# Performance work log

Measured on AMD Instinct MI355X. Metric: run time of the kernel, lower is better.

Reference implementation:

```python
import jax, jax.numpy as jnp
import numpy as np

B, N, D, H = 64, 196, 768, 3072
QMAX = 127.0  # 8-bit symmetric: clamp to [-128, 127]


def ste_round(x):
    # straight-through-estimator round (QAT)
    return x + jax.lax.stop_gradient(jnp.round(x) - x)


def q_linear_diag(x, w, b, a_sf):
    """Quantized diagonal linear (ResMLP Affine / LayerScale as QuantLinear)."""
    w_sf = jnp.max(jnp.abs(w)) / QMAX            # per-tensor weight scale
    w_int = ste_round(w / w_sf)                  # int8 weights (|.|<=127)
    out_int = (x / a_sf) * w_int
    if b is not None:
        out_int = out_int + ste_round(b / (a_sf * w_sf))  # 32-bit bias
    return out_int * (a_sf * w_sf), w_sf


def q_linear_dense(x, w, b, a_sf):
    """Quantized dense linear: int8 GEMM + int32 bias, dequant with a_sf*w_sf."""
    w_sf = jnp.max(jnp.abs(w)) / QMAX
    w_int = jnp.clip(ste_round(w / w_sf), -QMAX - 1, QMAX)
    out_int = jnp.einsum('...i,oi->...o', x / a_sf, w_int) + ste_round(b / (a_sf * w_sf))
    return out_int * (a_sf * w_sf), w_sf


def q_act(x, pre_sf, new_sf, identity=None, id_sf=None):
    """HAWQ-style QuantAct: fixed-point requantization to scale new_sf (8-bit)."""
    if identity is None:
        z_int = ste_round(x / pre_sf)
        out_int = ste_round(z_int * (pre_sf / new_sf))
    else:
        # main branch (x - identity) requantized with pre_sf, identity with id_sf
        z_int = ste_round((x - identity) / pre_sf)
        out_int = ste_round(z_int * (pre_sf / new_sf)) \
                + ste_round(ste_round(identity / id_sf) * (id_sf / new_sf))
    out_int = jnp.clip(out_int, -QMAX - 1, QMAX)
    return out_int * new_sf, new_sf


def _forward(x, norm1_w, norm1_b, attn_w, attn_b, gamma1_w,
             norm2_w, norm2_b, fc1_w, fc1_b, fc2_w, fc2_b, gamma2_w, act_sfs):
    a_sf = act_sfs[0]
    # --- token-mixing half ---
    identity, id_sf = x, a_sf
    x, w_sf = q_linear_diag(x, norm1_w, norm1_b, a_sf)         # norm1 (affine)
    x = jnp.swapaxes(x, 1, 2)                                  # [B, D, N]
    x, a_sf = q_act(x, a_sf * w_sf, act_sfs[1])                # quant_act1
    x, w_sf = q_linear_dense(x, attn_w, attn_b, a_sf)          # attn (cross-patch)
    x = jnp.swapaxes(x, 1, 2)                                  # [B, N, D]
    x, a_sf = q_act(x, a_sf * w_sf, act_sfs[2])                # quant_act2
    x, w_sf = q_linear_diag(x, gamma1_w, None, a_sf)           # gamma_1 (layerscale)
    x = x + identity
    x, a_sf = q_act(x, a_sf * w_sf, act_sfs[3], identity, id_sf)  # quant_act_int32_1
    # --- MLP half ---
    identity, id_sf = x, a_sf
    x, w_sf = q_linear_diag(x, norm2_w, norm2_b, a_sf)         # norm2
    x, a_sf = q_act(x, a_sf * w_sf, act_sfs[4])                # quant_act3
    x, w_sf = q_linear_dense(x, fc1_w, fc1_b, a_sf)            # mlp.fc1
    x = jax.nn.relu(x)
    x, a_sf = q_act(x, a_sf * w_sf, act_sfs[5])                # mlp.quant_act1
    x, w_sf = q_linear_dense(x, fc2_w, fc2_b, a_sf)            # mlp.fc2
    x, a_sf = q_act(x, a_sf * w_sf, act_sfs[6])                # mlp.quant_act2
    x, w_sf = q_linear_diag(x, gamma2_w, None, a_sf)           # gamma_2
    x = x + identity
    x, a_sf = q_act(x, a_sf * w_sf, act_sfs[7], identity, id_sf)  # quant_act_int32_2
    return x, a_sf


def setup_inputs() -> dict:
    key = jax.random.key(0)
    ks = jax.random.split(key, 16)
    act_sfs = jax.random.uniform(ks[14], (8,), jnp.float32, 0.02, 0.06)
    x = jax.random.normal(ks[0], (B, N, D), jnp.float32)
    # input is already quantized at scale act_sfs[0]
    x = jnp.clip(jnp.round(x / act_sfs[0]), -128, 127) * act_sfs[0]
    s = 0.05
    return {
        'x': x,
        'norm1_w': 1.0 + s * jax.random.normal(ks[1], (D,), jnp.float32),
        'norm1_b': s * jax.random.normal(ks[2], (D,), jnp.float32),
        'attn_w': jax.random.normal(ks[3], (N, N), jnp.float32) / np.sqrt(N),
        'attn_b': s * jax.random.normal(ks[4], (N,), jnp.float32),
        'gamma1_w': 0.1 + s * jax.random.normal(ks[5], (D,), jnp.float32),
        'norm2_w': 1.0 + s * jax.random.normal(ks[6], (D,), jnp.float32),
        'norm2_b': s * jax.random.normal(ks[7], (D,), jnp.float32),
        'fc1_w': jax.random.normal(ks[8], (H, D), jnp.float32) / np.sqrt(D),
        'fc1_b': s * jax.random.normal(ks[9], (H,), jnp.float32),
        'fc2_w': jax.random.normal(ks[10], (D, H), jnp.float32) / np.sqrt(H),
        'fc2_b': s * jax.random.normal(ks[11], (D,), jnp.float32),
        'gamma2_w': 0.1 + s * jax.random.normal(ks[12], (D,), jnp.float32),
        'act_sfs': act_sfs,
    }


def reference(x, norm1_w, norm1_b, attn_w, attn_b, gamma1_w,
              norm2_w, norm2_b, fc1_w, fc1_b, fc2_w, fc2_b, gamma2_w, act_sfs):
    return _forward(x, norm1_w, norm1_b, attn_w, attn_b, gamma1_w,
                    norm2_w, norm2_b, fc1_w, fc1_b, fc2_w, fc2_b, gamma2_w, act_sfs)
```

## Files before the change

kernel.cpp:

```cpp
#include <hip/hip_runtime.h>

#define B_ 64
#define N_ 196
#define D_ 768
#define H_ 3072
#define M_ (B_*N_)
#define NP 256

typedef int int4v __attribute__((ext_vector_type(4)));
typedef signed char i8;

#define WS_MAX 0
#define WS_W1F 16
#define WS_B1F (16+768)
#define WS_G1F (16+768*2)
#define WS_W2F (16+768*3)
#define WS_B2F (16+768*4)
#define WS_G2F (16+768*5)
#define WS_BA  (16+768*6)
#define WS_BF1 (WS_BA+256)
#define WS_BF2 (WS_BF1+3072)
#define OFF_WA   40960ull
#define OFF_FC1  (OFF_WA+65536ull)
#define OFF_FC2  (OFF_FC1+2359296ull)
#define OFF_X2   (OFF_FC2+2359296ull)
#define OFF_Q3   (OFF_X2+9633792ull)
#define OFF_Q4   (OFF_Q3+9633792ull)
#define OFF_Q1T  OFF_Q4
#define OFF_X8   (OFF_Q4+12582912ull)

__device__ __forceinline__ float clamp8(float v){ return fminf(fmaxf(v,-128.f),127.f); }

__device__ __forceinline__ void async16(const void* g, void* l){
    __builtin_amdgcn_global_load_lds((const __attribute__((address_space(1))) void*)g,
                                     (__attribute__((address_space(3))) void*)l, 16, 0, 0);
}

__global__ void k_init(char* ws, const float* __restrict__ act, float* out_tail){
    int id = blockIdx.x*256 + threadIdx.x;
    if (blockIdx.x == 0){
        float* f = (float*)ws;
        if (threadIdx.x < 8) f[WS_MAX+threadIdx.x] = 0.f;
        if (threadIdx.x == 8) *out_tail = act[7];
    }
    if (id < 4096){ int4v z = {0,0,0,0}; ((int4v*)(ws+OFF_WA))[id] = z; }
}

__global__ void k_maxabs(const float* __restrict__ p0, const float* __restrict__ p1,
                         const float* __restrict__ p2, const float* __restrict__ p3,
                         const float* __restrict__ p4, const float* __restrict__ p5,
                         const float* __restrict__ p6, float* wsmax){
    const float* ps[7] = {p0,p1,p2,p3,p4,p5,p6};
    const int    n4s[7] = {192, 9604, 192, 192, 589824, 589824, 192};
    int tid = blockIdx.y;
    const float4* p = (const float4*)ps[tid]; int n4 = n4s[tid];
    float m = 0.f;
    for (int i = blockIdx.x*blockDim.x + threadIdx.x; i < n4; i += gridDim.x*blockDim.x){
        float4 v = p[i];
        m = fmaxf(m, fmaxf(fmaxf(fabsf(v.x),fabsf(v.y)), fmaxf(fabsf(v.z),fabsf(v.w))));
    }
    #pragma unroll
    for (int off = 32; off; off >>= 1) m = fmaxf(m, __shfl_down(m, off, 64));
    __shared__ float red[4];
    int lane = threadIdx.x & 63, wv = threadIdx.x >> 6;
    if (lane == 0) red[wv] = m;
    __syncthreads();
    if (threadIdx.x == 0){
        float mm = red[0];
        for (int w = 1; w < (int)blockDim.x/64; w++) mm = fmaxf(mm, red[w]);
        atomicMax((unsigned*)&wsmax[tid], __float_as_uint(mm));
    }
}

__device__ __forceinline__ size_t cm_off(int o, int k, int KC){
    return (((size_t)(o>>7)*KC + (k>>6))<<13) + (((k>>4)&3)<<11) + ((o&127)<<4) + (k&15);
}

__global__ void k_qweights(const float* __restrict__ n1w, const float* __restrict__ n1b,
                           const float* __restrict__ aw,  const float* __restrict__ ab,
                           const float* __restrict__ g1w, const float* __restrict__ n2w,
                           const float* __restrict__ n2b, const float* __restrict__ f1w,
                           const float* __restrict__ f1b, const float* __restrict__ f2w,
                           const float* __restrict__ f2b, const float* __restrict__ g2w,
                           const float* __restrict__ act, char* ws){
    float* fws = (float*)ws;
    int*   iws = (int*)ws;
    const float* mx = fws + WS_MAX;
    long i = (long)blockIdx.x*blockDim.x + threadIdx.x;
    const long F4 = 589824;
    if (i < F4){ float sf = mx[4]/127.0f;
        float4 v = ((const float4*)f1w)[i];
        int o = (int)(i/192), kb = (int)(i%192)*4;
        unsigned b0 = (unsigned)(unsigned char)(i8)(int)fminf(fmaxf(rintf(v.x/sf),-128.f),127.f);
        unsigned b1 = (unsigned)(unsigned char)(i8)(int)fminf(fmaxf(rintf(v.y/sf),-128.f),127.f);
        unsigned b2 = (unsigned)(unsigned char)(i8)(int)fminf(fmaxf(rintf(v.z/sf),-128.f),127.f);
        unsigned b3 = (unsigned)(unsigned char)(i8)(int)fminf(fmaxf(rintf(v.w/sf),-128.f),127.f);
        *(unsigned*)(ws + OFF_FC1 + cm_off(o, kb, 12)) = b0 | (b1<<8) | (b2<<16) | (b3<<24);
        return; }
    i -= F4;
    if (i < F4){ float sf = mx[5]/127.0f;
        float4 v = ((const float4*)f2w)[i];
        int o = (int)(i/768), kb = (int)(i%768)*4;
        unsigned b0 = (unsigned)(unsigned char)(i8)(int)fminf(fmaxf(rintf(v.x/sf),-128.f),127.f);
        unsigned b1 = (unsigned)(unsigned char)(i8)(int)fminf(fmaxf(rintf(v.y/sf),-128.f),127.f);
        unsigned b2 = (unsigned)(unsigned char)(i8)(int)fminf(fmaxf(rintf(v.z/sf),-128.f),127.f);
        unsigned b3 = (unsigned)(unsigned char)(i8)(int)fminf(fmaxf(rintf(v.w/sf),-128.f),127.f);
        *(unsigned*)(ws + OFF_FC2 + cm_off(o, kb, 48)) = b0 | (b1<<8) | (b2<<16) | (b3<<24);
        return; }
    i -= F4;
    if (i < 38416){ float sf = mx[1]/127.0f;
        int o = (int)(i/196), k = (int)(i%196);
        ((i8*)(ws+OFF_WA))[cm_off(o, k, 4)] =
            (i8)(int)fminf(fmaxf(rintf(aw[i]/sf),-128.f),127.f); return; }
    i -= 38416;
    if (i < 768){ float sf = mx[0]/127.0f; fws[WS_W1F+i] = rintf(n1w[i]/sf); return; }
    i -= 768;
    if (i < 768){ float sf = mx[0]/127.0f; fws[WS_B1F+i] = rintf(n1b[i]/(act[0]*sf)); return; }
    i -= 768;
    if (i < 768){ float sf = mx[2]/127.0f; fws[WS_G1F+i] = rintf(g1w[i]/sf); return; }
    i -= 768;
    if (i < 768){ float sf = mx[3]/127.0f; fws[WS_W2F+i] = rintf(n2w[i]/sf); return; }
    i -= 768;
    if (i < 768){ float sf = mx[3]/127.0f; fws[WS_B2F+i] = rintf(n2b[i]/(act[3]*sf)); return; }
    i -= 768;
    if (i < 768){ float sf = mx[6]/127.0f; fws[WS_G2F+i] = rintf(g2w[i]/sf); return; }
    i -= 768;
    if (i < 196){ float sf = mx[1]/127.0f; iws[WS_BA+i] = (int)rintf(ab[i]/(act[1]*sf)); return; }
    i -= 196;
    if (i < 3072){ float sf = mx[4]/127.0f; iws[WS_BF1+i] = (int)rintf(f1b[i]/(act[4]*sf)); return; }
    i -= 3072;
    if (i < 768){ float sf = mx[5]/127.0f; iws[WS_BF2+i] = (int)rintf(f2b[i]/(act[5]*sf)); return; }
}

__global__ __launch_bounds__(256) void k_stage1(const float* __restrict__ x,
                                                const char* __restrict__ wsc,
                                                char* __restrict__ ws,
                                                const float* __restrict__ act){
    __shared__ i8 T[64][68];
    const float* fws = (const float*)wsc;
    int b = blockIdx.z, n0 = blockIdx.y*64, d0 = blockIdx.x*64;
    int t = threadIdx.x;
    float a0 = act[0];
    float w1sf = fws[WS_MAX+0]/127.0f;
    float r1 = (a0*w1sf)/act[1];
    int dl = (t & 15) * 4;
    int d  = d0 + dl;
    float4 wv = *(const float4*)(fws + WS_W1F + d);
    float4 bv = *(const float4*)(fws + WS_B1F + d);
    i8* x8 = (i8*)(ws + OFF_X8);
    #pragma unroll
    for (int pass = 0; pass < 4; pass++){
        int nl = (t >> 4) + pass*16;
        int n  = n0 + nl;
        i8 q[4] = {0,0,0,0};
        if (n < 196){
            float4 xv = *(const float4*)(x + ((size_t)b*196 + n)*768 + d);
            float i0 = rintf(xv.x/a0), i1 = rintf(xv.y/a0);
            float i2 = rintf(xv.z/a0), i3 = rintf(xv.w/a0);
            *(char4*)(x8 + ((size_t)b*196 + n)*768 + d) =
                make_char4((i8)(int)i0,(i8)(int)i1,(i8)(int)i2,(i8)(int)i3);
            float o0 = rintf(i0*wv.x + bv.x);
            float o1 = rintf(i1*wv.y + bv.y);
            float o2 = rintf(i2*wv.z + bv.z);
            float o3 = rintf(i3*wv.w + bv.w);
            q[0] = (i8)(int)clamp8(rintf(o0*r1));
            q[1] = (i8)(int)clamp8(rintf(o1*r1));
            q[2] = (i8)(int)clamp8(rintf(o2*r1));
            q[3] = (i8)(int)clamp8(rintf(o3*r1));
        }
        T[dl+0][nl] = q[0]; T[dl+1][nl] = q[1];
        T[dl+2][nl] = q[2]; T[dl+3][nl] = q[3];
    }
    __syncthreads();
    i8* q1T = (i8*)(ws + OFF_Q1T) + (size_t)b*196608;
    #pragma unroll
    for (int e = 0; e < 4; e++){
        int id = t + e*256;
        int row = id >> 4, c = (id & 15) * 4;
        int dd = d0 + row;
        int v = *(const int*)&T[row][c];
        size_t dst = (((size_t)(dd>>7)*4 + blockIdx.y)<<13) + ((size_t)(c>>4)<<11)
                     + ((dd&127)<<4) + (c&15);
        *(int*)(q1T + dst) = v;
    }
}

__device__ __forceinline__ void gemm_cm_512(const i8* __restrict__ gA, const i8* __restrict__ gB,
                                            int iters, int4v acc[4][2], i8* As, i8* Bs, int t){
    int lane = t & 63;
    int w = t >> 6, wm = w & 1, wn = w >> 1;
    int lo = t*16;
    async16(gA + lo, As + lo);
    async16(gB + lo, Bs + lo);
    int arow = (lane>>4)*2048 + (wm*64 + (lane&15))*16;
    int brow = (lane>>4)*2048 + (wn*32 + (lane&15))*16;
    for (int i = 0; i < iters; i++){
        __syncthreads();
        if (i+1 < iters){
            int nb = ((i+1)&1) << 13;
            size_t kb = (size_t)(i+1) << 13;
            async16(gA + kb + lo, As + nb + lo);
            async16(gB + kb + lo, Bs + nb + lo);
        }
        int cb = (i&1) << 13;
        int4v a[4], bb[2];
        #pragma unroll
        for (int mt = 0; mt < 4; mt++)
            a[mt] = *(const int4v*)(As + cb + arow + mt*256);
        #pragma unroll
        for (int nt = 0; nt < 2; nt++)
            bb[nt] = *(const int4v*)(Bs + cb + brow + nt*256);
        #pragma unroll
        for (int mt = 0; mt < 4; mt++)
            #pragma unroll
            for (int nt = 0; nt < 2; nt++)
                acc[mt][nt] = __builtin_amdgcn_mfma_i32_16x16x64_i8(a[mt], bb[nt], acc[mt][nt], 0,0,0);
    }
}

__device__ __forceinline__ void gemm_cm_256(const i8* __restrict__ gA, const i8* __restrict__ gB,
                                            int iters, int4v acc[4][4], i8* As, i8* Bs, int t){
    int lane = t & 63;
    int wm = (t>>6)&1, wn = t>>7;
    int lo = t*16;
    async16(gA + lo,        As + lo);
    async16(gA + 4096 + lo, As + 4096 + lo);
    async16(gB + lo,        Bs + lo);
    async16(gB + 4096 + lo, Bs + 4096 + lo);
    int arow = (lane>>4)*2048 + (wm*64 + (lane&15))*16;
    int brow = (lane>>4)*2048 + (wn*64 + (lane&15))*16;
    for (int i = 0; i < iters; i++){
        __syncthreads();
        if (i+1 < iters){
            int nb = ((i+1)&1) << 13;
            size_t kb = (size_t)(i+1) << 13;
            async16(gA + kb + lo,        As + nb + lo);
            async16(gA + kb + 4096 + lo, As + nb + 4096 + lo);
            async16(gB + kb + lo,        Bs + nb + lo);
            async16(gB + kb + 4096 + lo, Bs + nb + 4096 + lo);
        }
        int cb = (i&1) << 13;
        int4v a[4], bb[4];
        #pragma unroll
        for (int mt = 0; mt < 4; mt++)
            a[mt] = *(const int4v*)(As + cb + arow + mt*256);
        #pragma unroll
        for (int nt = 0; nt < 4; nt++)
            bb[nt] = *(const int4v*)(Bs + cb + brow + nt*256);
        #pragma unroll
        for (int mt = 0; mt < 4; mt++)
            #pragma unroll
            for (int nt = 0; nt < 4; nt++)
                acc[mt][nt] = __builtin_amdgcn_mfma_i32_16x16x64_i8(a[mt], bb[nt], acc[mt][nt], 0,0,0);
    }
}

__global__ __launch_bounds__(256) void k_attn(const char* __restrict__ ws,
                                              const float* __restrict__ act){
    __shared__ char smem[32768];
    const float* fws = (const float*)ws;
    const int*   iws = (const int*)ws;
    int b = blockIdx.z;
    int m0 = blockIdx.x*128, n0 = blockIdx.y*128;
    const i8* gA = (const i8*)(ws + OFF_WA)  + ((size_t)(m0>>7))*32768;
    const i8* gB = (const i8*)(ws + OFF_Q1T) + (size_t)b*196608 + ((size_t)(n0>>7))*32768;
    const i8* x8 = (const i8*)(ws + OFF_X8);
    i8* x2  = (i8*)(ws + OFF_X2);
    i8* q3  = (i8*)(ws + OFF_Q3);
    int t = threadIdx.x, lane = t & 63;
    int wm = (t>>6)&1, wn = t>>7;
    int4v acc[4][4]; int4v zz = {0,0,0,0};
    #pragma unroll
    for (int mt=0;mt<4;mt++) for (int nt=0;nt<4;nt++) acc[mt][nt] = zz;
    gemm_cm_256(gA, gB, 4, acc, (i8*)smem, (i8*)smem+16384, t);

    float a1=act[1], a2=act[2], a3=act[3], a4=act[4];
    float wasf = fws[WS_MAX+1]/127.0f; float r2  = (a1*wasf)/a2;
    float g1sf = fws[WS_MAX+2]/127.0f; float r3a = (a2*g1sf)/a3; float r3b = act[0]/a3;
    float w2sf = fws[WS_MAX+3]/127.0f; float r4  = (a3*w2sf)/a4;
    float g1v[4], w2v[4], b2v[4];
    #pragma unroll
    for (int nt=0;nt<4;nt++){
        int d = n0 + wn*64 + nt*16 + (lane&15);
        g1v[nt] = fws[WS_G1F + d]; w2v[nt] = fws[WS_W2F + d]; b2v[nt] = fws[WS_B2F + d];
    }
    __syncthreads();
    i8* Xs = (i8*)smem;
    i8* Qs = (i8*)smem + 16384;
    #pragma unroll
    for (int mt=0;mt<4;mt++){
        #pragma unroll
        for (int r=0;r<4;r++){
            int ml = wm*64 + mt*16 + (lane>>4)*4 + r;
            int o  = m0 + ml;
            int ba = iws[WS_BA + o];
            #pragma unroll
            for (int nt=0;nt<4;nt++){
                int nl = wn*64 + nt*16 + (lane&15);
                int d  = n0 + nl;
                float s2 = (float)(acc[mt][nt][r] + ba);
                float q2 = clamp8(rintf(s2*r2));
                float o3v = q2*g1v[nt];
                float idi = (o < 196) ? (float)x8[((size_t)b*196 + o)*768 + d] : 0.f;
                float tt = rintf(o3v*r3a) + rintf(idi*r3b);
                tt = clamp8(tt);
                float o4 = tt*w2v[nt] + b2v[nt];
                float qr = clamp8(rintf(o4*r4));
                Xs[ml*128 + nl] = (i8)(int)tt;
                Qs[ml*128 + nl] = (i8)(int)qr;
            }
        }
    }
    __syncthreads();
    #pragma unroll
    for (int e=0;e<4;e++){
        int id = t + e*256;
        int row = id>>3, c = id&7;
        int o = m0 + row;
        if (o < 196){
            int rg = b*196 + o;
            size_t g = (size_t)rg*768 + n0 + c*16;
            *(int4v*)(x2 + g) = *(const int4v*)(Xs + row*128 + c*16);
            size_t dst = (((size_t)(rg>>7)*12 + (n0>>6) + (c>>2))<<13)
                         + ((size_t)(c&3)<<11) + ((rg&127)<<4);
            *(int4v*)(q3 + dst) = *(const int4v*)(Qs + row*128 + c*16);
        }
    }
}

__global__ __launch_bounds__(512) void k_fc1(const char* __restrict__ ws, const float* __restrict__ act){
    __shared__ char smem[32768];
    const float* fws = (const float*)ws;
    const int*   iws = (const int*)ws;
    int m0 = blockIdx.x*128, n0 = blockIdx.y*128;
    const i8* gA = (const i8*)(ws+OFF_Q3)  + ((size_t)blockIdx.x)*12*8192;
    const i8* gB = (const i8*)(ws+OFF_FC1) + ((size_t)blockIdx.y)*12*8192;
    const int* bias = iws + WS_BF1;
    i8* q4 = (i8*)(ws+OFF_Q4);
    int t = threadIdx.x, lane = t & 63;
    int w = t >> 6, wm = w & 1, wn = w >> 1;
    int4v acc[4][2]; int4v zz = {0,0,0,0};
    #pragma unroll
    for (int mt=0;mt<4;mt++) for (int nt=0;nt<2;nt++) acc[mt][nt] = zz;
    gemm_cm_512(gA, gB, 12, acc, (i8*)smem, (i8*)smem+16384, t);
    float wsf = fws[WS_MAX+4]/127.0f;
    float r5 = (act[4]*wsf)/act[5];
    int bcol[2];
    #pragma unroll
    for (int nt=0;nt<2;nt++) bcol[nt] = bias[n0 + wn*32 + nt*16 + (lane&15)];
    __syncthreads();
    i8* Cs = (i8*)smem;
    #pragma unroll
    for (int mt=0;mt<4;mt++){
        #pragma unroll
        for (int nt=0;nt<2;nt++){
            int nl = wn*32 + nt*16 + (lane&15);
            #pragma unroll
            for (int r=0;r<4;r++){
                int s = acc[mt][nt][r] + bcol[nt];
                if (s < 0) s = 0;
                float q = clamp8(rintf((float)s * r5));
                int ml = wm*64 + mt*16 + (lane>>4)*4 + r;
                Cs[ml*128 + nl] = (i8)(int)q;
            }
        }
    }
    __syncthreads();
    #pragma unroll
    for (int e=0;e<2;e++){
        int id = t + e*512;
        int row = id>>3, c = id&7;
        size_t dst = (((size_t)blockIdx.x*48 + (n0>>6) + (c>>2))<<13)
                     + ((size_t)(c&3)<<11) + ((size_t)row<<4);
        *(int4v*)(q4 + dst) = *(const int4v*)(Cs + row*128 + c*16);
    }
}

__global__ __launch_bounds__(512) void k_fc2(const char* __restrict__ ws, const float* __restrict__ act,
                                             float* __restrict__ out){
    __shared__ char smem[32768];
    const float* fws = (const float*)ws;
    const int*   iws = (const int*)ws;
    int m0 = blockIdx.x*128, n0 = blockIdx.y*128;
    const i8* gA = (const i8*)(ws+OFF_Q4)  + ((size_t)blockIdx.x)*48*8192;
    const i8* gB = (const i8*)(ws+OFF_FC2) + ((size_t)blockIdx.y)*48*8192;
    const int* bias = iws + WS_BF2;
    const float* g2f = fws + WS_G2F;
    const i8* x2 = (const i8*)(ws+OFF_X2);
    int t = threadIdx.x, lane = t & 63;
    int w = t >> 6, wm = w & 1, wn = w >> 1;
    int4v acc[4][2]; int4v zz = {0,0,0,0};
    #pragma unroll
    for (int mt=0;mt<4;mt++) for (int nt=0;nt<2;nt++) acc[mt][nt] = zz;
    gemm_cm_512(gA, gB, 48, acc, (i8*)smem, (i8*)smem+16384, t);
    float a3=act[3], a5=act[5], a6=act[6], a7=act[7];
    float wsf  = fws[WS_MAX+5]/127.0f; float r6  = (a5*wsf)/a6;
    float g2sf = fws[WS_MAX+6]/127.0f; float r7a = (a6*g2sf)/a7; float r7b = a3/a7;
    int bcol[2]; float g2v[2];
    #pragma unroll
    for (int nt=0;nt<2;nt++){
        int nc = n0 + wn*32 + nt*16 + (lane&15);
        bcol[nt] = bias[nc]; g2v[nt] = g2f[nc];
    }
    #pragma unroll
    for (int mt=0;mt<4;mt++){
        #pragma unroll
        for (int nt=0;nt<2;nt++){
            int nc = n0 + wn*32 + nt*16 + (lane&15);
            #pragma unroll
            for (int r=0;r<4;r++){
                int ml = wm*64 + mt*16 + (lane>>4)*4 + r;
                size_t gi = (size_t)(m0+ml)*768 + nc;
                int s = acc[mt][nt][r] + bcol[nt];
                float q6 = clamp8(rintf((float)s*r6));
                float o7 = q6*g2v[nt];
                float idi = (float)x2[gi];
                float tt = rintf(o7*r7a) + rintf(idi*r7b);
                tt = clamp8(tt);
                out[gi] = tt*a7;
            }
        }
    }
}

extern "C" void kernel_launch(void* const* d_in, const int* in_sizes, int n_in,
                              void* d_out, int out_size, void* d_ws, size_t ws_size,
                              hipStream_t stream){
    const float* x   = (const float*)d_in[0];
    const float* n1w = (const float*)d_in[1];
    const float* n1b = (const float*)d_in[2];
    const float* aw  = (const float*)d_in[3];
    const float* ab  = (const float*)d_in[4];
    const float* g1w = (const float*)d_in[5];
    const float* n2w = (const float*)d_in[6];
    const float* n2b = (const float*)d_in[7];
    const float* f1w = (const float*)d_in[8];
    const float* f1b = (const float*)d_in[9];
    const float* f2w = (const float*)d_in[10];
    const float* f2b = (const float*)d_in[11];
    const float* g2w = (const float*)d_in[12];
    const float* act = (const float*)d_in[13];
    char* ws = (char*)d_ws;
    float* out = (float*)d_out;

    k_init<<<16,256,0,stream>>>(ws, act, out + (size_t)B_*N_*D_);
    k_maxabs<<<dim3(120,7),256,0,stream>>>(n1w, aw, g1w, n2w, f1w, f2w, g2w, (float*)ws);
    long qwThreads = 2L*589824 + 38416 + 768L*6 + 196 + 3072 + 768;
    k_qweights<<<(int)((qwThreads+255)/256),256,0,stream>>>(n1w,n1b,aw,ab,g1w,n2w,n2b,
                                                            f1w,f1b,f2w,f2b,g2w,act,ws);
    k_stage1<<<dim3(12,4,64),256,0,stream>>>(x, ws, ws, act);
    k_attn<<<dim3(2,6,64),256,0,stream>>>(ws, act);
    k_fc1<<<dim3(98,24),512,0,stream>>>(ws, act);
    k_fc2<<<dim3(98,6),512,0,stream>>>(ws, act, out);
}
```

Baseline: 266.3 us.

## Switch FC GEMMs to 32x32x32 int8 MFMA with 256-thread blocks

Replaces the 512-thread 16x16x64 MFMA GEMM used by fc1 and fc2 with a 256-thread version built on 32x32x32 int8 MFMA. Each wave now computes a 64x64 tile as 2x2 32x32 blocks, taking two K sub-steps per 64-wide K chunk, and the epilogue index mapping changes to match the 32x32 accumulator layout. The aim is fewer LDS fragment reads per MAC and better MFMA throughput per wave. The cost is more accumulator registers per thread and half as many waves per block, which could reduce latency hiding.

```diff
diff --git a/kernel.cpp b/kernel.cpp
--- a/kernel.cpp
+++ b/kernel.cpp
@@ -7,7 +7,8 @@
 #define M_ (B_*N_)
 #define NP 256
 
-typedef int int4v __attribute__((ext_vector_type(4)));
+typedef int int4v  __attribute__((ext_vector_type(4)));
+typedef int int16v __attribute__((ext_vector_type(16)));
 typedef signed char i8;
 
 #define WS_MAX 0
@@ -185,39 +186,6 @@
     }
 }
 
-__device__ __forceinline__ void gemm_cm_512(const i8* __restrict__ gA, const i8* __restrict__ gB,
-                                            int iters, int4v acc[4][2], i8* As, i8* Bs, int t){
-    int lane = t & 63;
-    int w = t >> 6, wm = w & 1, wn = w >> 1;
-    int lo = t*16;
-    async16(gA + lo, As + lo);
-    async16(gB + lo, Bs + lo);
-    int arow = (lane>>4)*2048 + (wm*64 + (lane&15))*16;
-    int brow = (lane>>4)*2048 + (wn*32 + (lane&15))*16;
-    for (int i = 0; i < iters; i++){
-        __syncthreads();
-        if (i+1 < iters){
-            int nb = ((i+1)&1) << 13;
-            size_t kb = (size_t)(i+1) << 13;
-            async16(gA + kb + lo, As + nb + lo);
-            async16(gB + kb + lo, Bs + nb + lo);
-        }
-        int cb = (i&1) << 13;
-        int4v a[4], bb[2];
-        #pragma unroll
-        for (int mt = 0; mt < 4; mt++)
-            a[mt] = *(const int4v*)(As + cb + arow + mt*256);
-        #pragma unroll
-        for (int nt = 0; nt < 2; nt++)
-            bb[nt] = *(const int4v*)(Bs + cb + brow + nt*256);
-        #pragma unroll
-        for (int mt = 0; mt < 4; mt++)
-            #pragma unroll
-            for (int nt = 0; nt < 2; nt++)
-                acc[mt][nt] = __builtin_amdgcn_mfma_i32_16x16x64_i8(a[mt], bb[nt], acc[mt][nt], 0,0,0);
-    }
-}
-
 __device__ __forceinline__ void gemm_cm_256(const i8* __restrict__ gA, const i8* __restrict__ gB,
                                             int iters, int4v acc[4][4], i8* As, i8* Bs, int t){
     int lane = t & 63;
@@ -255,6 +223,47 @@
     }
 }
 
+__device__ __forceinline__ void gemm32_cm_256(const i8* __restrict__ gA, const i8* __restrict__ gB,
+                                              int iters, int16v acc[2][2], i8* As, i8* Bs, int t){
+    int lane = t & 63;
+    int wm = (t>>6)&1, wn = t>>7;
+    int lo = t*16;
+    async16(gA + lo,        As + lo);
+    async16(gA + 4096 + lo, As + 4096 + lo);
+    async16(gB + lo,        Bs + lo);
+    async16(gB + 4096 + lo, Bs + 4096 + lo);
+    int arow = (lane>>5)*2048 + (wm*64 + (lane&31))*16;
+    int brow = (lane>>5)*2048 + (wn*64 + (lane&31))*16;
+    for (int i = 0; i < iters; i++){
+        __syncthreads();
+        if (i+1 < iters){
+            int nb = ((i+1)&1) << 13;
+            size_t kb = (size_t)(i+1) << 13;
+            async16(gA + kb + lo,        As + nb + lo);
+            async16(gA + kb + 4096 + lo, As + nb + 4096 + lo);
+            async16(gB + kb + lo,        Bs + nb + lo);
+            async16(gB + kb + 4096 + lo, Bs + nb + 4096 + lo);
+        }
+        int cb = (i&1) << 13;
+        int4v a[2][2], bb[2][2];
+        #pragma unroll
+        for (int kk = 0; kk < 2; kk++){
+            #pragma unroll
+            for (int mt = 0; mt < 2; mt++){
+                a[kk][mt]  = *(const int4v*)(As + cb + kk*4096 + arow + mt*512);
+                bb[kk][mt] = *(const int4v*)(Bs + cb + kk*4096 + brow + mt*512);
+            }
+        }
+        #pragma unroll
+        for (int mt = 0; mt < 2; mt++)
+            #pragma unroll
+            for (int nt = 0; nt < 2; nt++)
+                #pragma unroll
+                for (int kk = 0; kk < 2; kk++)
+                    acc[mt][nt] = __builtin_amdgcn_mfma_i32_32x32x32_i8(a[kk][mt], bb[kk][nt], acc[mt][nt], 0,0,0);
+    }
+}
+
 __global__ __launch_bounds__(256) void k_attn(const char* __restrict__ ws,
                                               const float* __restrict__ act){
     __shared__ char smem[32768];
@@ -328,47 +337,48 @@
     }
 }
 
-__global__ __launch_bounds__(512) void k_fc1(const char* __restrict__ ws, const float* __restrict__ act){
+__global__ __launch_bounds__(256,4) void k_fc1(const char* __restrict__ ws, const float* __restrict__ act){
     __shared__ char smem[32768];
     const float* fws = (const float*)ws;
     const int*   iws = (const int*)ws;
-    int m0 = blockIdx.x*128, n0 = blockIdx.y*128;
+    int n0 = blockIdx.y*128;
     const i8* gA = (const i8*)(ws+OFF_Q3)  + ((size_t)blockIdx.x)*12*8192;
     const i8* gB = (const i8*)(ws+OFF_FC1) + ((size_t)blockIdx.y)*12*8192;
     const int* bias = iws + WS_BF1;
     i8* q4 = (i8*)(ws+OFF_Q4);
     int t = threadIdx.x, lane = t & 63;
-    int w = t >> 6, wm = w & 1, wn = w >> 1;
-    int4v acc[4][2]; int4v zz = {0,0,0,0};
-    #pragma unroll
-    for (int mt=0;mt<4;mt++) for (int nt=0;nt<2;nt++) acc[mt][nt] = zz;
-    gemm_cm_512(gA, gB, 12, acc, (i8*)smem, (i8*)smem+16384, t);
+    int wm = (t>>6)&1, wn = t>>7;
+    int16v acc[2][2];
+    int16v zz = {0,0,0,0,0,0,0,0,0,0,0,0,0,0,0,0};
+    #pragma unroll
+    for (int mt=0;mt<2;mt++) for (int nt=0;nt<2;nt++) acc[mt][nt] = zz;
+    gemm32_cm_256(gA, gB, 12, acc, (i8*)smem, (i8*)smem+16384, t);
     float wsf = fws[WS_MAX+4]/127.0f;
     float r5 = (act[4]*wsf)/act[5];
     int bcol[2];
     #pragma unroll
-    for (int nt=0;nt<2;nt++) bcol[nt] = bias[n0 + wn*32 + nt*16 + (lane&15)];
+    for (int nt=0;nt<2;nt++) bcol[nt] = bias[n0 + wn*64 + nt*32 + (lane&31)];
     __syncthreads();
     i8* Cs = (i8*)smem;
     #pragma unroll
-    for (int mt=0;mt<4;mt++){
+    for (int mt=0;mt<2;mt++){
         #pragma unroll
         for (int nt=0;nt<2;nt++){
-            int nl = wn*32 + nt*16 + (lane&15);
-            #pragma unroll
-            for (int r=0;r<4;r++){
+            int nl = wn*64 + nt*32 + (lane&31);
+            #pragma unroll
+            for (int r=0;r<16;r++){
                 int s = acc[mt][nt][r] + bcol[nt];
                 if (s < 0) s = 0;
                 float q = clamp8(rintf((float)s * r5));
-                int ml = wm*64 + mt*16 + (lane>>4)*4 + r;
+                int ml = wm*64 + mt*32 + 4*(lane>>5) + (r&3) + 8*(r>>2);
                 Cs[ml*128 + nl] = (i8)(int)q;
             }
         }
     }
     __syncthreads();
     #pragma unroll
-    for (int e=0;e<2;e++){
-        int id = t + e*512;
+    for (int e=0;e<4;e++){
+        int id = t + e*256;
         int row = id>>3, c = id&7;
         size_t dst = (((size_t)blockIdx.x*48 + (n0>>6) + (c>>2))<<13)
                      + ((size_t)(c&3)<<11) + ((size_t)row<<4);
@@ -376,8 +386,8 @@
     }
 }
 
-__global__ __launch_bounds__(512) void k_fc2(const char* __restrict__ ws, const float* __restrict__ act,
-                                             float* __restrict__ out){
+__global__ __launch_bounds__(256,4) void k_fc2(const char* __restrict__ ws, const float* __restrict__ act,
+                                               float* __restrict__ out){
     __shared__ char smem[32768];
     const float* fws = (const float*)ws;
     const int*   iws = (const int*)ws;
@@ -388,28 +398,29 @@
     const float* g2f = fws + WS_G2F;
     const i8* x2 = (const i8*)(ws+OFF_X2);
     int t = threadIdx.x, lane = t & 63;
-    int w = t >> 6, wm = w & 1, wn = w >> 1;
-    int4v acc[4][2]; int4v zz = {0,0,0,0};
-    #pragma unroll
-    for (int mt=0;mt<4;mt++) for (int nt=0;nt<2;nt++) acc[mt][nt] = zz;
-    gemm_cm_512(gA, gB, 48, acc, (i8*)smem, (i8*)smem+16384, t);
+    int wm = (t>>6)&1, wn = t>>7;
+    int16v acc[2][2];
+    int16v zz = {0,0,0,0,0,0,0,0,0,0,0,0,0,0,0,0};
+    #pragma unroll
+    for (int mt=0;mt<2;mt++) for (int nt=0;nt<2;nt++) acc[mt][nt] = zz;
+    gemm32_cm_256(gA, gB, 48, acc, (i8*)smem, (i8*)smem+16384, t);
     float a3=act[3], a5=act[5], a6=act[6], a7=act[7];
     float wsf  = fws[WS_MAX+5]/127.0f; float r6  = (a5*wsf)/a6;
     float g2sf = fws[WS_MAX+6]/127.0f; float r7a = (a6*g2sf)/a7; float r7b = a3/a7;
     int bcol[2]; float g2v[2];
     #pragma unroll
     for (int nt=0;nt<2;nt++){
-        int nc = n0 + wn*32 + nt*16 + (lane&15);
+        int nc = n0 + wn*64 + nt*32 + (lane&31);
         bcol[nt] = bias[nc]; g2v[nt] = g2f[nc];
     }
     #pragma unroll
-    for (int mt=0;mt<4;mt++){
+    for (int mt=0;mt<2;mt++){
         #pragma unroll
         for (int nt=0;nt<2;nt++){
-            int nc = n0 + wn*32 + nt*16 + (lane&15);
-            #pragma unroll
-            for (int r=0;r<4;r++){
-                int ml = wm*64 + mt*16 + (lane>>4)*4 + r;
+            int nc = n0 + wn*64 + nt*32 + (lane&31);
+            #pragma unroll
+            for (int r=0;r<16;r++){
+                int ml = wm*64 + mt*32 + 4*(lane>>5) + (r&3) + 8*(r>>2);
                 size_t gi = (size_t)(m0+ml)*768 + nc;
                 int s = acc[mt][nt][r] + bcol[nt];
                 float q6 = clamp8(rintf((float)s*r6));
@@ -450,6 +461,6 @@
                                                             f1w,f1b,f2w,f2b,g2w,act,ws);
     k_stage1<<<dim3(12,4,64),256,0,stream>>>(x, ws, ws, act);
     k_attn<<<dim3(2,6,64),256,0,stream>>>(ws, act);
-    k_fc1<<<dim3(98,24),512,0,stream>>>(ws, act);
-    k_fc2<<<dim3(98,6),512,0,stream>>>(ws, act, out);
-}
+    k_fc1<<<dim3(98,24),256,0,stream>>>(ws, act);
+    k_fc2<<<dim3(98,6),256,0,stream>>>(ws, act, out);
+}
```

Result: no change. 261.8 us (-1.7%).
